# Performance work log

Measured on AMD Instinct MI355X. Metric: run time of the kernel, lower is better.

## Reference

```python
import jax, jax.numpy as jnp
import numpy as np

EPS = 1e-5

def conv3x3(x, w, b):
    # x: [B,C,H,W], w: [O,I,3,3], padding=1 (SAME)
    y = jax.lax.conv_general_dilated(x, w, window_strides=(1, 1),
                                     padding=[(1, 1), (1, 1)],
                                     dimension_numbers=('NCHW', 'OIHW', 'NCHW'))
    return y + b[None, :, None, None]

def pool_block(x, k):
    # exact adaptive avg pool: 300 is divisible by the output size, block size k
    B, C, H, W = x.shape
    return x.reshape(B, C, H // k, k, W // k, k).mean(axis=(3, 5))

def upsample_nearest(x, k):
    # equivalent to the nested python-loop slice-assign in RIA
    return jnp.repeat(jnp.repeat(x, k, axis=2), k, axis=3)

def _conv_param(key, o, i):
    k1, k2 = jax.random.split(key)
    fan_in = i * 9
    w = jax.random.normal(k1, (o, i, 3, 3), jnp.float32) * np.sqrt(2.0 / fan_in)
    b = jax.random.normal(k2, (o,), jnp.float32) * 0.01
    return w, b

def setup_inputs() -> dict:
    key = jax.random.key(0)
    ks = jax.random.split(key, 16)
    inp = {}
    inp['im'] = jax.random.normal(ks[0], (32, 3, 300, 300), jnp.float32)
    inp['w1'], inp['b1'] = _conv_param(ks[1], 8, 3)
    inp['w2'], inp['b2'] = _conv_param(ks[2], 16, 8)
    inp['w3'], inp['b3'] = _conv_param(ks[3], 32, 16)
    inp['w4'], inp['b4'] = _conv_param(ks[4], 16, 32)
    inp['w5'], inp['b5'] = _conv_param(ks[5], 8, 16)
    inp['wc5'], inp['bc5'] = _conv_param(ks[6], 8, 16)
    inp['wc10'], inp['bc10'] = _conv_param(ks[7], 8, 16)
    inp['wc15'], inp['bc15'] = _conv_param(ks[8], 8, 16)
    inp['wg'], inp['bg'] = _conv_param(ks[9], 8, 24)
    inp['wm'], inp['bm'] = _conv_param(ks[10], 8, 24)
    inp['bn_w'] = jnp.ones((8,), jnp.float32)
    inp['bn_b'] = jnp.zeros((8,), jnp.float32)
    inp['w11'], inp['b11'] = _conv_param(ks[11], 1, 8)
    inp['gamma'] = jnp.full((1,), 0.3, jnp.float32)
    return inp

def reference(im, w1, b1, w2, b2, w3, b3, w4, b4, w5, b5,
              wc5, bc5, wc10, bc10, wc15, bc15,
              wg, bg, wm, bm, bn_w, bn_b, w11, b11, gamma):
    # attention conv chain 3->8->16->32->16->8
    x = conv3x3(im, w1, b1)
    x = conv3x3(x, w2, b2)
    x = conv3x3(x, w3, b3)
    x = conv3x3(x, w4, b4)
    x = conv3x3(x, w5, b5)  # [B,8,300,300]

    # RIA: triple-scale pooled context, nearest-upsampled and fused
    up5 = upsample_nearest(pool_block(x, 5), 5)
    up10 = upsample_nearest(pool_block(x, 10), 10)
    up15 = upsample_nearest(pool_block(x, 15), 15)
    c5 = conv3x3(jnp.concatenate([x, up5], axis=1), wc5, bc5)
    c10 = conv3x3(jnp.concatenate([x, up10], axis=1), wc10, bc10)
    c15 = conv3x3(jnp.concatenate([x, up15], axis=1), wc15, bc15)
    g_in = jnp.concatenate([c5, c10, c15], axis=1)  # [B,24,300,300]

    # gated conv (activation=None): conv(x) * sigmoid(mask_conv(x)), then BN (batch stats)
    gated = conv3x3(g_in, wg, bg) * jax.nn.sigmoid(conv3x3(g_in, wm, bm))
    mean = gated.mean(axis=(0, 2, 3), keepdims=True)
    var = gated.var(axis=(0, 2, 3), keepdims=True)
    gated = (gated - mean) * jax.lax.rsqrt(var + EPS)
    gated = gated * bn_w[None, :, None, None] + bn_b[None, :, None, None]

    # 8->1 conv, sigmoid attention map, residual gating with gamma
    att = jax.nn.sigmoid(conv3x3(gated, w11, b11))  # [B,1,300,300]
    out = gamma * (att * im) + (1.0 - gamma) * im
    return out
```

## Files before the change

kernel.cpp:

```cpp
#include <hip/hip_runtime.h>
#include <hip/hip_bf16.h>
#include <math.h>

typedef __hip_bfloat16 bf16;
typedef __attribute__((ext_vector_type(8))) __bf16 bf16x8;
typedef __attribute__((ext_vector_type(8))) unsigned short u16x8;
typedef __attribute__((ext_vector_type(4))) float f32x4;

#define H_ 300
#define W_ 300
#define HW_ 90000
#define NBATCH 32
#define NPART (NBATCH * 190)
#define NPB 95

__device__ __forceinline__ float b2f(unsigned short u) {
    return __uint_as_float((unsigned int)u << 16);
}
__device__ __forceinline__ unsigned short f2u(float v) {
    bf16 b = __float2bfloat16(v);
    return *reinterpret_cast<unsigned short*>(&b);
}
__device__ __forceinline__ float sigm(float x) { return 1.f / (1.f + __expf(-x)); }
__device__ __forceinline__ unsigned int packbf(float a, float b) {
    unsigned int r;
    asm("v_cvt_pk_bf16_f32 %0, %1, %2" : "=v"(r) : "v"(a), "v"(b));
    return r;
}
__device__ __forceinline__ void async_cp16(void* lds_base, const void* g) {
    __builtin_amdgcn_global_load_lds(
        (const __attribute__((address_space(1))) unsigned int*)g,
        (__attribute__((address_space(3))) unsigned int*)lds_base, 16, 0, 0);
}

__global__ void pack_all_k(
    const float* __restrict__ w1, const float* __restrict__ w2,
    const float* __restrict__ w3, const float* __restrict__ w4,
    const float* __restrict__ w5, const float* __restrict__ wc5,
    const float* __restrict__ wc10, const float* __restrict__ wc15,
    const float* __restrict__ wg, const float* __restrict__ wm,
    unsigned short* __restrict__ WP)
{
    const float *a = nullptr, *bsec = nullptr;
    int cs = 999, CO = 0, CI = 0, CP = 8, NS = 3, NG = 1, off = 0, special = 0;
    switch (blockIdx.x) {
        case 0: a = w2;  CO = 16; CI = 8;  CP = 8;  NS = 3; off = 0;     break;
        case 1: a = w3;  CO = 32; CI = 16; CP = 16; NS = 5; NG = 2; off = 2048;  break;
        case 2: a = w4;  CO = 16; CI = 32; CP = 32; NS = 9; off = 8192;  break;
        case 3: a = w5;  CO = 8;  CI = 16; CP = 16; NS = 5; off = 13312; break;
        case 4: special = 1; CO = 32; CI = 32; CP = 32; NS = 9; NG = 2;
                off = 16384; break;
        case 5: a = wg; bsec = wm; cs = 8; CO = 16; CI = 24; CP = 32; NS = 9;
                off = 25600; break;
        case 6: a = w1;  CO = 8;  CI = 3;  CP = 8;  NS = 3; off = 30720; break;
    }
    unsigned short* outp = WP + off;
    int TPK = 32 / CP;
    int total = NS * NG * 512;
    for (int idx = threadIdx.x; idx < total; idx += 256) {
        int j = idx & 7;
        int lane = (idx >> 3) & 63;
        int g = (idx >> 9) % NG;
        int s = idx / (512 * NG);
        int col = lane & 15, kg = lane >> 4;
        int kk = kg * 8 + j;
        int tt = kk / CP, ci = kk % CP;
        int tap = s * TPK + tt;
        float v = 0.f;
        if (special) {
            int o = ci >> 3, c8 = ci & 7;
            int convid = (g == 0) ? (col < 8 ? 0 : 1) : (col < 8 ? 2 : -1);
            if (tap < 9 && convid >= 0) {
                const float* wc = (convid == 0) ? wc5 : (convid == 1) ? wc10 : wc15;
                int colc = col & 7;
                if (o == 0) v = wc[(colc * 16 + c8) * 9 + tap];
                else if (o == convid + 1) v = wc[(colc * 16 + 8 + c8) * 9 + tap];
            }
        } else {
            int co = g * 16 + col;
            if (tap < 9 && ci < CI && co < CO)
                v = (co >= cs) ? bsec[((co - cs) * CI + ci) * 9 + tap]
                               : a[(co * CI + ci) * 9 + tap];
        }
        outp[idx] = f2u(v);
    }
}

template <int CIN, int CINP, int COUT, int NGI, int MODE, int TH>
__global__ __launch_bounds__(256) void mfconv_k(
    const unsigned short* __restrict__ src,
    const unsigned short* __restrict__ wpack,
    const float* __restrict__ bias0, const float* __restrict__ bias1,
    unsigned short* __restrict__ out, int co_total, int co_off,
    float2* __restrict__ bnp, int img_base)
{
    constexpr int TPK = 32 / CINP;
    constexpr int NSTEP = (9 + TPK - 1) / TPK;
    constexpr int OCT = CINP / 8;
    constexpr int NPX = (TH + 2) * 34;
    constexpr int STRIDE = 256 / OCT;

    __shared__ __align__(16) unsigned short s_in[OCT * NPX * 8];

    int b = blockIdx.z;
    int x0 = blockIdx.x * 32, y0 = blockIdx.y * TH;
    int tid = threadIdx.x;
    int lane = tid & 63, wv = tid >> 6;
    bool interior = (x0 >= 1) && (x0 + 32 < W_) && (y0 >= 1) && (y0 + TH < H_);

    int oct = (OCT == 1) ? 0 : (wv % OCT);
    int phase = (OCT == 4) ? 0 : (wv / OCT);
    bool voct = (CIN == CINP) || (oct * 8 < CIN);

    if (MODE == 3) {
        const float* sf = reinterpret_cast<const float*>(src) + (size_t)b * 3 * HW_;
        if (interior) {
            const float* sf0 = sf + (size_t)(y0 - 1) * W_ + (x0 - 1);
            for (int e = tid; e < NPX; e += 256) {
                int y = e / 34;
                size_t o = (size_t)e + (size_t)y * 266;
                u16x8 v = {0, 0, 0, 0, 0, 0, 0, 0};
                v[0] = f2u(sf0[o]);
                v[1] = f2u(sf0[HW_ + o]);
                v[2] = f2u(sf0[2 * HW_ + o]);
                *(u16x8*)&s_in[e * 8] = v;
            }
        } else {
            for (int e = tid; e < NPX; e += 256) {
                int y = e / 34, x = e - y * 34;
                int gy = y0 + y - 1, gx = x0 + x - 1;
                u16x8 v = {0, 0, 0, 0, 0, 0, 0, 0};
                if (gy >= 0 && gy < H_ && gx >= 0 && gx < W_) {
                    size_t o = (size_t)gy * W_ + gx;
                    v[0] = f2u(sf[o]);
                    v[1] = f2u(sf[HW_ + o]);
                    v[2] = f2u(sf[2 * HW_ + o]);
                }
                *(u16x8*)&s_in[e * 8] = v;
            }
        }
    } else {
        const unsigned short* sb = src + (size_t)b * CIN * HW_;
        if (interior) {
            if (voct) {
                const unsigned short* sb0 =
                    sb + ((size_t)(y0 - 1) * W_ + (x0 - 1)) * CIN + oct * 8;
#pragma unroll
                for (int pxb = 0; pxb < NPX; pxb += STRIDE) {
                    int base = phase * 64 + pxb;
                    if (base >= NPX) break;
                    int px = base + lane;
                    if (px < NPX) {
                        int y = px / 34;
                        async_cp16(&s_in[(oct * NPX + base) * 8],
                                   &sb0[(size_t)(px + y * 266) * CIN]);
                    }
                }
            } else {
                u16x8 z8 = {0, 0, 0, 0, 0, 0, 0, 0};
                for (int px = lane + phase * 64; px < NPX; px += STRIDE)
                    *(u16x8*)&s_in[(oct * NPX + px) * 8] = z8;
            }
        } else {
            for (int px = lane + phase * 64; px < NPX; px += STRIDE) {
                int y = px / 34, x = px - y * 34;
                int gy = y0 + y - 1, gx = x0 + x - 1;
                u16x8 v = {0, 0, 0, 0, 0, 0, 0, 0};
                if (gy >= 0 && gy < H_ && gx >= 0 && gx < W_ && voct)
                    v = *(const u16x8*)&sb[((size_t)gy * W_ + gx) * CIN + oct * 8];
                *(u16x8*)&s_in[(oct * NPX + px) * 8] = v;
            }
        }
    }

    bf16x8 bw[NGI][NSTEP];
#pragma unroll
    for (int gi = 0; gi < NGI; ++gi)
#pragma unroll
        for (int s = 0; s < NSTEP; ++s)
            bw[gi][s] = *(const bf16x8*)&wpack[((s * NGI + gi) * 64 + lane) * 8];

    int col = lane & 15, kg = lane >> 4;

    float bias_r[NGI][4];
#pragma unroll
    for (int gi = 0; gi < NGI; ++gi)
#pragma unroll
        for (int r = 0; r < 4; ++r) {
            if (MODE == 2)
                bias_r[0][r] = (kg < 2) ? bias0[kg * 4 + r] : bias1[(kg - 2) * 4 + r];
            else {
                int co_l = gi * 16 + kg * 4 + r;
                bias_r[gi][r] = (co_l < COUT) ? bias0[co_l] : 0.f;
            }
        }

    float bs[4] = {0.f, 0.f, 0.f, 0.f}, bs2[4] = {0.f, 0.f, 0.f, 0.f};

    __syncthreads();

    if constexpr (OCT == 4) {
        int myb = wv * (TH / 4);
#pragma unroll
        for (int tx = 0; tx < 2; ++tx) {
            int pbase = kg * NPX + tx * 16 + col;
            bf16x8 fr[3][3];
#pragma unroll
            for (int r = 0; r < 2; ++r)
#pragma unroll
                for (int dx = 0; dx < 3; ++dx)
                    fr[r][dx] =
                        *(const bf16x8*)&s_in[(pbase + (myb + r) * 34 + dx) * 8];
#pragma unroll
            for (int ii = 0; ii < TH / 4; ++ii) {
#pragma unroll
                for (int dx = 0; dx < 3; ++dx)
                    fr[(ii + 2) % 3][dx] =
                        *(const bf16x8*)&s_in[(pbase + (myb + ii + 2) * 34 + dx) * 8];

                f32x4 acc[NGI];
#pragma unroll
                for (int gi = 0; gi < NGI; ++gi) acc[gi] = {0.f, 0.f, 0.f, 0.f};
#pragma unroll
                for (int dy = 0; dy < 3; ++dy)
#pragma unroll
                    for (int dx = 0; dx < 3; ++dx) {
                        bf16x8 a = fr[(ii + dy) % 3][dx];
#pragma unroll
                        for (int gi = 0; gi < NGI; ++gi)
                            acc[gi] = __builtin_amdgcn_mfma_f32_16x16x32_bf16(
                                bw[gi][dy * 3 + dx], a, acc[gi], 0, 0, 0);
                    }

                int gy = y0 + myb + ii;
                int gxx = x0 + tx * 16 + col;
                if (gy < H_) {
                    if (MODE == 2) {
                        float v0 = acc[0].x + bias_r[0][0];
                        float v1 = acc[0].y + bias_r[0][1];
                        float v2 = acc[0].z + bias_r[0][2];
                        float v3 = acc[0].w + bias_r[0][3];
                        float m0 = __shfl_xor(v0, 32), m1 = __shfl_xor(v1, 32);
                        float m2 = __shfl_xor(v2, 32), m3 = __shfl_xor(v3, 32);
                        if (kg < 2 && gxx < W_) {
                            float o0 = v0 * sigm(m0), o1 = v1 * sigm(m1);
                            float o2 = v2 * sigm(m2), o3 = v3 * sigm(m3);
                            uint2 st;
                            st.x = packbf(o0, o1);
                            st.y = packbf(o2, o3);
                            *(uint2*)&out[(((size_t)b * HW_ + (size_t)gy * W_ +
                                            gxx) * 8) + kg * 4] = st;
                            bs[0] += o0; bs2[0] += o0 * o0;
                            bs[1] += o1; bs2[1] += o1 * o1;
                            bs[2] += o2; bs2[2] += o2 * o2;
                            bs[3] += o3; bs2[3] += o3 * o3;
                        }
                    } else {
#pragma unroll
                        for (int gi = 0; gi < NGI; ++gi) {
                            int co_g = gi * 16 + kg * 4;
                            if (co_g < COUT && gxx < W_) {
                                uint2 st;
                                st.x = packbf(acc[gi].x + bias_r[gi][0],
                                              acc[gi].y + bias_r[gi][1]);
                                st.y = packbf(acc[gi].z + bias_r[gi][2],
                                              acc[gi].w + bias_r[gi][3]);
                                *(uint2*)&out[((size_t)b * HW_ +
                                               (size_t)gy * W_ + gxx) *
                                                  co_total + co_off + co_g] = st;
                            }
                        }
                    }
                }
            }
        }
    } else {
        int offs[NSTEP];
#pragma unroll
        for (int s = 0; s < NSTEP; ++s) {
            int t = s * TPK + kg / OCT;
            if (t > 8) t = 8;
            offs[s] = ((t / 3) * 34 + (t % 3)) * 8 + (kg % OCT) * (NPX * 8);
        }

#pragma unroll
        for (int i = 0; i < TH / 2; ++i) {
            int m = wv * (TH / 2) + i;
            int my = m >> 1, tx = m & 1;
            int gy = y0 + my;
            if (gy >= H_) continue;
            int base = (my * 34 + tx * 16 + col) * 8;

            f32x4 acc[NGI];
#pragma unroll
            for (int gi = 0; gi < NGI; ++gi) acc[gi] = {0.f, 0.f, 0.f, 0.f};
#pragma unroll
            for (int s = 0; s < NSTEP; ++s) {
                bf16x8 a = *(const bf16x8*)&s_in[base + offs[s]];
#pragma unroll
                for (int gi = 0; gi < NGI; ++gi)
                    acc[gi] = __builtin_amdgcn_mfma_f32_16x16x32_bf16(
                        bw[gi][s], a, acc[gi], 0, 0, 0);
            }

            int gxx = x0 + tx * 16 + col;
#pragma unroll
            for (int gi = 0; gi < NGI; ++gi) {
                int co_g = gi * 16 + kg * 4;
                if (co_g < COUT && gxx < W_) {
                    uint2 st;
                    st.x = packbf(acc[gi].x + bias_r[gi][0],
                                  acc[gi].y + bias_r[gi][1]);
                    st.y = packbf(acc[gi].z + bias_r[gi][2],
                                  acc[gi].w + bias_r[gi][3]);
                    *(uint2*)&out[((size_t)b * HW_ + (size_t)gy * W_ + gxx) *
                                      co_total + co_off + co_g] = st;
                }
            }
        }
    }

    if constexpr (MODE == 2) {
#pragma unroll
        for (int off = 1; off < 16; off <<= 1) {
#pragma unroll
            for (int r = 0; r < 4; ++r) {
                bs[r] += __shfl_xor(bs[r], off);
                bs2[r] += __shfl_xor(bs2[r], off);
            }
        }
        __shared__ float bsum[4][8], bsq[4][8];
        if (lane == 0) {
#pragma unroll
            for (int r = 0; r < 4; ++r) { bsum[wv][r] = bs[r]; bsq[wv][r] = bs2[r]; }
        }
        if (lane == 16) {
#pragma unroll
            for (int r = 0; r < 4; ++r) {
                bsum[wv][4 + r] = bs[r];
                bsq[wv][4 + r] = bs2[r];
            }
        }
        __syncthreads();
        if (tid < 8) {
            float s = 0.f, s2 = 0.f;
#pragma unroll
            for (int w = 0; w < 4; ++w) { s += bsum[w][tid]; s2 += bsq[w][tid]; }
            int bIdx = (img_base + b) * 190 + blockIdx.y * 10 + blockIdx.x;
            bnp[(size_t)bIdx * 8 + tid] = make_float2(s, s2);
        }
    }
}

__global__ __launch_bounds__(256) void convc3_k(
    const unsigned short* __restrict__ src,
    const unsigned short* __restrict__ p5, const unsigned short* __restrict__ p10,
    const unsigned short* __restrict__ p15,
    const unsigned short* __restrict__ wpack,
    const float* __restrict__ bc5, const float* __restrict__ bc10,
    const float* __restrict__ bc15, unsigned short* __restrict__ out)
{
    constexpr int TH = 16;
    constexpr int NPX = (TH + 2) * 34;
    __shared__ __align__(16) unsigned short s_in[4 * NPX * 8];

    int b = blockIdx.z;
    int x0 = blockIdx.x * 32, y0 = blockIdx.y * TH;
    int tid = threadIdx.x;
    int lane = tid & 63, wv = tid >> 6;
    bool interior = (x0 >= 1) && (x0 + 32 < W_) && (y0 >= 1) && (y0 + TH < H_);

    const unsigned short* sb = src + (size_t)b * 8 * HW_;
    const unsigned short* pb5 = p5 + (size_t)b * 8 * 3600;
    const unsigned short* pb10 = p10 + (size_t)b * 8 * 900;
    const unsigned short* pb15 = p15 + (size_t)b * 8 * 400;

    int oct = wv;
    if (interior) {
        if (oct == 0) {
            const unsigned short* sb0 =
                sb + ((size_t)(y0 - 1) * W_ + (x0 - 1)) * 8;
#pragma unroll
            for (int base = 0; base < NPX; base += 64) {
                int px = base + lane;
                if (px < NPX) {
                    int y = px / 34;
                    async_cp16(&s_in[(size_t)base * 8],
                               &sb0[(size_t)(px + y * 266) * 8]);
                }
            }
        } else {
            for (int px = lane; px < NPX; px += 64) {
                int y = px / 34, x = px - y * 34;
                int gy = y0 - 1 + y, gx = x0 - 1 + x;
                const unsigned short* pp =
                    (oct == 1) ? &pb5[((size_t)(gy / 5) * 60 + gx / 5) * 8]
                    : (oct == 2) ? &pb10[((size_t)(gy / 10) * 30 + gx / 10) * 8]
                                 : &pb15[((size_t)(gy / 15) * 20 + gx / 15) * 8];
                *(u16x8*)&s_in[(oct * NPX + px) * 8] = *(const u16x8*)pp;
            }
        }
    } else {
        for (int px = lane; px < NPX; px += 64) {
            int y = px / 34, x = px - y * 34;
            int gy = y0 + y - 1, gx = x0 + x - 1;
            u16x8 v = {0, 0, 0, 0, 0, 0, 0, 0};
            if (gy >= 0 && gy < H_ && gx >= 0 && gx < W_) {
                if (oct == 0)
                    v = *(const u16x8*)&sb[((size_t)gy * W_ + gx) * 8];
                else if (oct == 1)
                    v = *(const u16x8*)&pb5[((size_t)(gy / 5) * 60 + gx / 5) * 8];
                else if (oct == 2)
                    v = *(const u16x8*)&pb10[((size_t)(gy / 10) * 30 + gx / 10) * 8];
                else
                    v = *(const u16x8*)&pb15[((size_t)(gy / 15) * 20 + gx / 15) * 8];
            }
            *(u16x8*)&s_in[(oct * NPX + px) * 8] = v;
        }
    }

    bf16x8 bw[2][9];
#pragma unroll
    for (int g = 0; g < 2; ++g)
#pragma unroll
        for (int s = 0; s < 9; ++s)
            bw[g][s] = *(const bf16x8*)&wpack[((s * 2 + g) * 64 + lane) * 8];

    int col = lane & 15, kg = lane >> 4;
    float bias_r[2][4];
#pragma unroll
    for (int r = 0; r < 4; ++r) {
        bias_r[0][r] = (kg < 2) ? bc5[kg * 4 + r] : bc10[(kg - 2) * 4 + r];
        bias_r[1][r] = (kg < 2) ? bc15[kg * 4 + r] : 0.f;
    }

    __syncthreads();

    int myb = wv * (TH / 4);
#pragma unroll
    for (int tx = 0; tx < 2; ++tx) {
        int pbase = kg * NPX + tx * 16 + col;
        bf16x8 fr[3][3];
#pragma unroll
        for (int r = 0; r < 2; ++r)
#pragma unroll
            for (int dx = 0; dx < 3; ++dx)
                fr[r][dx] = *(const bf16x8*)&s_in[(pbase + (myb + r) * 34 + dx) * 8];
#pragma unroll
        for (int ii = 0; ii < TH / 4; ++ii) {
#pragma unroll
            for (int dx = 0; dx < 3; ++dx)
                fr[(ii + 2) % 3][dx] =
                    *(const bf16x8*)&s_in[(pbase + (myb + ii + 2) * 34 + dx) * 8];

            f32x4 acc[2];
            acc[0] = {0.f, 0.f, 0.f, 0.f};
            acc[1] = {0.f, 0.f, 0.f, 0.f};
#pragma unroll
            for (int dy = 0; dy < 3; ++dy)
#pragma unroll
                for (int dx = 0; dx < 3; ++dx) {
                    bf16x8 a = fr[(ii + dy) % 3][dx];
                    acc[0] = __builtin_amdgcn_mfma_f32_16x16x32_bf16(
                        bw[0][dy * 3 + dx], a, acc[0], 0, 0, 0);
                    acc[1] = __builtin_amdgcn_mfma_f32_16x16x32_bf16(
                        bw[1][dy * 3 + dx], a, acc[1], 0, 0, 0);
                }

            int gy = y0 + myb + ii;
            int gxx = x0 + tx * 16 + col;
            if (gy < H_ && gxx < W_) {
                size_t pxo = ((size_t)b * HW_ + (size_t)gy * W_ + gxx) * 24;
                uint2 st0;
                st0.x = packbf(acc[0].x + bias_r[0][0], acc[0].y + bias_r[0][1]);
                st0.y = packbf(acc[0].z + bias_r[0][2], acc[0].w + bias_r[0][3]);
                *(uint2*)&out[pxo + kg * 4] = st0;
                if (kg < 2) {
                    uint2 st1;
                    st1.x = packbf(acc[1].x + bias_r[1][0], acc[1].y + bias_r[1][1]);
                    st1.y = packbf(acc[1].z + bias_r[1][2], acc[1].w + bias_r[1][3]);
                    *(uint2*)&out[pxo + 16 + kg * 4] = st1;
                }
            }
        }
    }
}

__global__ __launch_bounds__(256) void pool5_k(const unsigned short* __restrict__ x,
                                               unsigned short* __restrict__ p5,
                                               int n)
{
    int idx = blockIdx.x * 256 + threadIdx.x;
    if (idx >= n) return;
    int b = idx / 3600;
    int rem = idx - b * 3600;
    int i = rem / 60, j = rem - i * 60;
    const unsigned short* src =
        x + ((size_t)b * HW_ + (size_t)(i * 5) * W_ + j * 5) * 8;
    float ss[8] = {0, 0, 0, 0, 0, 0, 0, 0};
#pragma unroll
    for (int r = 0; r < 5; ++r)
#pragma unroll
        for (int c = 0; c < 5; ++c) {
            u16x8 v = *(const u16x8*)&src[((size_t)r * W_ + c) * 8];
#pragma unroll
            for (int k = 0; k < 8; ++k) ss[k] += b2f(v[k]);
        }
    uint4 st;
    st.x = packbf(ss[0] * 0.04f, ss[1] * 0.04f);
    st.y = packbf(ss[2] * 0.04f, ss[3] * 0.04f);
    st.z = packbf(ss[4] * 0.04f, ss[5] * 0.04f);
    st.w = packbf(ss[6] * 0.04f, ss[7] * 0.04f);
    *(uint4*)&p5[(size_t)idx * 8] = st;
}

template <int R, int OD>
__device__ __forceinline__ void poolr_body(const unsigned short* __restrict__ p5,
                                           unsigned short* __restrict__ po, int idx)
{
    int b = idx / (OD * OD);
    int rem = idx - b * OD * OD;
    int i = rem / OD, j = rem - i * OD;
    const unsigned short* src =
        p5 + ((size_t)b * 3600 + (size_t)(i * R) * 60 + j * R) * 8;
    float ss[8] = {0, 0, 0, 0, 0, 0, 0, 0};
    const float inv = 1.f / (R * R);
#pragma unroll
    for (int r = 0; r < R; ++r)
#pragma unroll
        for (int c = 0; c < R; ++c) {
            u16x8 v = *(const u16x8*)&src[((size_t)r * 60 + c) * 8];
#pragma unroll
            for (int k = 0; k < 8; ++k) ss[k] += b2f(v[k]);
        }
    uint4 st;
    st.x = packbf(ss[0] * inv, ss[1] * inv);
    st.y = packbf(ss[2] * inv, ss[3] * inv);
    st.z = packbf(ss[4] * inv, ss[5] * inv);
    st.w = packbf(ss[6] * inv, ss[7] * inv);
    *(uint4*)&po[(size_t)idx * 8] = st;
}

__global__ __launch_bounds__(256) void poolrs_k(const unsigned short* __restrict__ p5,
                                                unsigned short* __restrict__ p10,
                                                unsigned short* __restrict__ p15,
                                                int n10, int n15)
{
    int idx = blockIdx.x * 256 + threadIdx.x;
    if (idx < n10) {
        poolr_body<2, 30>(p5, p10, idx);
    } else {
        idx -= n10;
        if (idx < n15) poolr_body<3, 20>(p5, p15, idx);
    }
}

__global__ __launch_bounds__(256) void reduce_parts_k(
    const float2* __restrict__ parts, float2* __restrict__ parts2)
{
    int k = blockIdx.x;
    int tid = threadIdx.x;
    int c = tid & 7, j = tid >> 3;
    float s = 0.f, s2 = 0.f;
    for (int r = j; r < NPB; r += 32) {
        float2 p = parts[((size_t)k * NPB + r) * 8 + c];
        s += p.x;
        s2 += p.y;
    }
    __shared__ float2 red[256];
    red[tid] = make_float2(s, s2);
    __syncthreads();
    if (tid < 8) {
        float a = 0.f, b = 0.f;
        for (int q = 0; q < 32; ++q) {
            float2 p = red[q * 8 + tid];
            a += p.x;
            b += p.y;
        }
        parts2[(size_t)k * 8 + tid] = make_float2(a, b);
    }
}

__global__ __launch_bounds__(256) void stats_fold_k(
    const float2* __restrict__ parts2, const float* __restrict__ bn_w,
    const float* __restrict__ bn_b, const float* __restrict__ w11,
    const float* __restrict__ b11, float* __restrict__ wfold)
{
    __shared__ float sc[8], tc[8];
    __shared__ float2 acc8[8];
    int tid = threadIdx.x;
    int c = tid >> 5, sl = tid & 31;
    float s = 0.f, s2 = 0.f;
    for (int i = sl; i < 64; i += 32) {
        float2 p = parts2[(size_t)i * 8 + c];
        s += p.x;
        s2 += p.y;
    }
#pragma unroll
    for (int off = 16; off > 0; off >>= 1) {
        s += __shfl_down(s, off, 32);
        s2 += __shfl_down(s2, off, 32);
    }
    if (sl == 0) acc8[c] = make_float2(s, s2);
    __syncthreads();
    if (tid < 8) {
        double ds = acc8[tid].x, ds2 = acc8[tid].y;
        double N = (double)NBATCH * HW_;
        double mean = ds / N;
        double var = ds2 / N - mean * mean;
        float rstd = (float)(1.0 / sqrt(var + 1e-5));
        float scv = bn_w[tid] * rstd;
        sc[tid] = scv;
        tc[tid] = bn_b[tid] - (float)mean * scv;
    }
    __syncthreads();
    if (tid < 72) {
        int t = tid >> 3, ci = tid & 7;
        wfold[tid] = w11[ci * 9 + t] * sc[ci];
    }
    if (tid == 72) {
        float a = b11[0];
        for (int i = 0; i < 72; ++i) a += w11[i] * tc[i / 9];
        wfold[72] = a;
    }
}

__global__ __launch_bounds__(256) void final_k(
    const unsigned short* __restrict__ gated, const float* __restrict__ wf,
    const float* __restrict__ im, const float* __restrict__ gamma,
    float* __restrict__ out)
{
    __shared__ __align__(16) unsigned short s_g[1156 * 8];
    __shared__ float s_w[80];

    int b = blockIdx.z;
    int x0 = blockIdx.x * 32, y0 = blockIdx.y * 32;
    int tid = threadIdx.x;
    bool interior = (x0 >= 1) && (x0 + 32 < W_) && (y0 >= 1) && (y0 + 32 < H_);

    if (tid < 73) s_w[tid] = wf[tid];

    const unsigned short* gb = gated + (size_t)b * HW_ * 8;
    if (interior) {
        const unsigned short* gb0 = gb + ((size_t)(y0 - 1) * W_ + (x0 - 1)) * 8;
        for (int e = tid; e < 1156; e += 256) {
            int y = e / 34;
            u16x8 v = *(const u16x8*)&gb0[(size_t)(e + y * 266) * 8];
            *(u16x8*)&s_g[e * 8] = v;
        }
    } else {
        for (int e = tid; e < 1156; e += 256) {
            int y = e / 34, x = e - y * 34;
            int gy = y0 + y - 1, gx = x0 + x - 1;
            u16x8 v = {0, 0, 0, 0, 0, 0, 0, 0};
            if (gy >= 0 && gy < H_ && gx >= 0 && gx < W_)
                v = *(const u16x8*)&gb[((size_t)gy * W_ + gx) * 8];
            *(u16x8*)&s_g[e * 8] = v;
        }
    }
    __syncthreads();

    int qx = (tid & 15) * 2, qy = (tid >> 4) * 2;
    float f[4];
    float gm = *gamma;
#pragma unroll
    for (int p = 0; p < 4; ++p) {
        int ly = qy + (p >> 1), lx = qx + (p & 1);
        float acc = s_w[72];
#pragma unroll
        for (int t = 0; t < 9; ++t) {
            u16x8 n = *(const u16x8*)&s_g[((ly + t / 3) * 34 + lx + t % 3) * 8];
#pragma unroll
            for (int ci = 0; ci < 8; ++ci) acc += b2f(n[ci]) * s_w[t * 8 + ci];
        }
        f[p] = (1.f - gm) + gm * sigm(acc);
    }

    int px = x0 + qx, py = y0 + qy;
    if (px < W_) {
#pragma unroll
        for (int ch = 0; ch < 3; ++ch) {
            const float* imb = im + ((size_t)b * 3 + ch) * HW_;
            float* ob = out + ((size_t)b * 3 + ch) * HW_;
#pragma unroll
            for (int pr = 0; pr < 2; ++pr) {
                if (py + pr < H_) {
                    float2 iv = *(const float2*)&imb[(size_t)(py + pr) * W_ + px];
                    float2 ov;
                    ov.x = iv.x * f[pr * 2 + 0];
                    ov.y = iv.y * f[pr * 2 + 1];
                    *(float2*)&ob[(size_t)(py + pr) * W_ + px] = ov;
                }
            }
        }
    }
}


extern "C" void kernel_launch(void* const* d_in, const int* in_sizes, int n_in,
                              void* d_out, int out_size, void* d_ws,
                              size_t ws_size, hipStream_t stream)
{
    (void)in_sizes; (void)n_in; (void)out_size;

    const float* im  = (const float*)d_in[0];
    const float* w1  = (const float*)d_in[1];
    const float* b1  = (const float*)d_in[2];
    const float* w2  = (const float*)d_in[3];
    const float* b2  = (const float*)d_in[4];
    const float* w3  = (const float*)d_in[5];
    const float* b3  = (const float*)d_in[6];
    const float* w4  = (const float*)d_in[7];
    const float* b4  = (const float*)d_in[8];
    const float* w5  = (const float*)d_in[9];
    const float* b5  = (const float*)d_in[10];
    const float* wc5 = (const float*)d_in[11];
    const float* bc5 = (const float*)d_in[12];
    const float* wc10= (const float*)d_in[13];
    const float* bc10= (const float*)d_in[14];
    const float* wc15= (const float*)d_in[15];
    const float* bc15= (const float*)d_in[16];
    const float* wg  = (const float*)d_in[17];
    const float* bg  = (const float*)d_in[18];
    const float* wm  = (const float*)d_in[19];
    const float* bm  = (const float*)d_in[20];
    const float* bnw = (const float*)d_in[21];
    const float* bnb = (const float*)d_in[22];
    const float* w11 = (const float*)d_in[23];
    const float* b11 = (const float*)d_in[24];
    const float* gam = (const float*)d_in[25];
    float* out = (float*)d_out;

    const size_t GATED_B = 46080000;
    const size_t PER_IMG = 1440000 + 2880000 + 5760000 + 57600 + 14400 + 6656;
    const size_t MISC    = 1048576;
    int c = 32;
    while (c > 1 && GATED_B + MISC + (size_t)c * PER_IMG + 2048 > ws_size)
        c >>= 1;

    char* p = (char*)d_ws;
    auto take = [&](size_t bytes) {
        char* r = p;
        p += (bytes + 255) & ~(size_t)255;
        return r;
    };
    unsigned short* GATED = (unsigned short*)take(GATED_B);
    unsigned short* A   = (unsigned short*)take((size_t)c * 1440000);
    unsigned short* Bb  = (unsigned short*)take((size_t)c * 2880000);
    unsigned short* C   = (unsigned short*)take((size_t)c * 5760000);
    unsigned short* P5  = (unsigned short*)take((size_t)c * 57600);
    unsigned short* P10 = (unsigned short*)take((size_t)c * 14400);
    unsigned short* P15 = (unsigned short*)take((size_t)c * 6656);
    float2* parts  = (float2*)take((size_t)NPART * 8 * sizeof(float2));
    float2* parts2 = (float2*)take(64 * 8 * sizeof(float2));
    float*  wfold  = (float*)take(512);
    unsigned short* WP = (unsigned short*)take(65536);

    unsigned short* PK2 = WP;
    unsigned short* PK3 = WP + 2048;
    unsigned short* PK4 = WP + 8192;
    unsigned short* PK5 = WP + 13312;
    unsigned short* PKc = WP + 16384;
    unsigned short* PKg = WP + 25600;
    unsigned short* PK1 = WP + 30720;

    dim3 blk(256);

    pack_all_k<<<dim3(7), blk, 0, stream>>>(w1, w2, w3, w4, w5, wc5, wc10, wc15,
                                            wg, wm, WP);

    for (int b0 = 0; b0 < NBATCH; b0 += c) {
        dim3 g32(10, 10, c);
        dim3 g16(10, 19, c);
        const float* imc = im + (size_t)b0 * 3 * HW_;

        mfconv_k<8, 8, 8, 1, 3, 32><<<g32, blk, 0, stream>>>(
            (const unsigned short*)imc, PK1, b1, nullptr, A, 8, 0, nullptr, 0);
        mfconv_k<8, 8, 16, 1, 0, 32><<<g32, blk, 0, stream>>>(
            A, PK2, b2, nullptr, Bb, 16, 0, nullptr, 0);
        mfconv_k<16, 16, 32, 2, 0, 32><<<g32, blk, 0, stream>>>(
            Bb, PK3, b3, nullptr, C, 32, 0, nullptr, 0);
        mfconv_k<32, 32, 16, 1, 0, 16><<<g16, blk, 0, stream>>>(
            C, PK4, b4, nullptr, Bb, 16, 0, nullptr, 0);
        mfconv_k<16, 16, 8, 1, 0, 32><<<g32, blk, 0, stream>>>(
            Bb, PK5, b5, nullptr, A, 8, 0, nullptr, 0);

        int n5 = c * 3600, n10 = c * 900, n15 = c * 400;
        pool5_k<<<dim3((n5 + 255) / 256), blk, 0, stream>>>(A, P5, n5);
        poolrs_k<<<dim3((n10 + n15 + 255) / 256), blk, 0, stream>>>(P5, P10, P15,
                                                                    n10, n15);

        convc3_k<<<g16, blk, 0, stream>>>(A, P5, P10, P15, PKc, bc5, bc10, bc15, C);

        mfconv_k<24, 32, 16, 1, 2, 16><<<g16, blk, 0, stream>>>(
            C, PKg, bg, bm, GATED + (size_t)b0 * HW_ * 8, 8, 0, parts, b0);
    }

    reduce_parts_k<<<dim3(64), blk, 0, stream>>>(parts, parts2);
    stats_fold_k<<<dim3(1), blk, 0, stream>>>(parts2, bnw, bnb, w11, b11, wfold);
    final_k<<<dim3(10, 10, NBATCH), blk, 0, stream>>>(GATED, wfold, im, gam,
                                                      out);
}
```

Baseline: 419.1 us.

## Fuse first two convolutions into one kernel and async-load final_k tile

Adds a kernel that computes conv1 (3->8) on a halo-extended 34x34 tile in shared memory and then conv2 (8->16) from it. This removes the intermediate A write and read and one launch per chunk, at the cost of recomputing halo pixels of conv1. It also switches the interior tile load in final_k to async 16-byte copies and drops the now-unused float-input mode from mfconv_k.

```diff
diff --git a/kernel.cpp b/kernel.cpp
--- a/kernel.cpp
+++ b/kernel.cpp
@@ -86,6 +86,127 @@
     }
 }
 
+__global__ __launch_bounds__(256) void fused12_k(
+    const float* __restrict__ im, const unsigned short* __restrict__ wp1,
+    const float* __restrict__ b1, const unsigned short* __restrict__ wp2,
+    const float* __restrict__ b2, unsigned short* __restrict__ out)
+{
+    __shared__ __align__(16) unsigned short s_im[1296 * 8];
+    __shared__ __align__(16) unsigned short s_x1[1156 * 8];
+
+    int b = blockIdx.z;
+    int x0 = blockIdx.x * 32, y0 = blockIdx.y * 32;
+    int tid = threadIdx.x;
+    int lane = tid & 63, wv = tid >> 6;
+    int col = lane & 15, kg = lane >> 4;
+
+    const float* sf = im + (size_t)b * 3 * HW_;
+    bool interior = (x0 >= 2) && (x0 + 34 < W_) && (y0 >= 2) && (y0 + 34 < H_);
+    if (interior) {
+        const float* sf0 = sf + (size_t)(y0 - 2) * W_ + (x0 - 2);
+        for (int e = tid; e < 1296; e += 256) {
+            int y = e / 36;
+            size_t o = (size_t)e + (size_t)y * 264;
+            u16x8 v = {0, 0, 0, 0, 0, 0, 0, 0};
+            v[0] = f2u(sf0[o]);
+            v[1] = f2u(sf0[HW_ + o]);
+            v[2] = f2u(sf0[2 * HW_ + o]);
+            *(u16x8*)&s_im[e * 8] = v;
+        }
+    } else {
+        for (int e = tid; e < 1296; e += 256) {
+            int y = e / 36, x = e - y * 36;
+            int gy = y0 + y - 2, gx = x0 + x - 2;
+            u16x8 v = {0, 0, 0, 0, 0, 0, 0, 0};
+            if (gy >= 0 && gy < H_ && gx >= 0 && gx < W_) {
+                size_t o = (size_t)gy * W_ + gx;
+                v[0] = f2u(sf[o]);
+                v[1] = f2u(sf[HW_ + o]);
+                v[2] = f2u(sf[2 * HW_ + o]);
+            }
+            *(u16x8*)&s_im[e * 8] = v;
+        }
+    }
+
+    bf16x8 bw1[3], bw2[3];
+#pragma unroll
+    for (int s = 0; s < 3; ++s) {
+        bw1[s] = *(const bf16x8*)&wp1[(s * 64 + lane) * 8];
+        bw2[s] = *(const bf16x8*)&wp2[(s * 64 + lane) * 8];
+    }
+
+    int offs1[3], offs2[3];
+#pragma unroll
+    for (int s = 0; s < 3; ++s) {
+        int t = s * 4 + kg;
+        if (t > 8) t = 8;
+        offs1[s] = ((t / 3) * 36 + (t % 3)) * 8;
+        offs2[s] = ((t / 3) * 34 + (t % 3)) * 8;
+    }
+
+    float b1r[4], b2r[4];
+#pragma unroll
+    for (int r = 0; r < 4; ++r) {
+        int co1 = kg * 4 + r;
+        b1r[r] = (co1 < 8) ? b1[co1] : 0.f;
+        b2r[r] = b2[kg * 4 + r];
+    }
+
+    __syncthreads();
+
+    for (int r = wv; r < 34; r += 4) {
+#pragma unroll
+        for (int cg = 0; cg < 3; ++cg) {
+            int base = (r * 36 + cg * 16 + col) * 8;
+            f32x4 acc = {0.f, 0.f, 0.f, 0.f};
+#pragma unroll
+            for (int s = 0; s < 3; ++s) {
+                bf16x8 a = *(const bf16x8*)&s_im[base + offs1[s]];
+                acc = __builtin_amdgcn_mfma_f32_16x16x32_bf16(bw1[s], a, acc, 0, 0, 0);
+            }
+            int c = cg * 16 + col;
+            if (kg < 2 && c < 34) {
+                int gy = y0 - 1 + r, gx = x0 - 1 + c;
+                bool ok = (gy >= 0) && (gy < H_) && (gx >= 0) && (gx < W_);
+                float o0 = ok ? acc.x + b1r[0] : 0.f;
+                float o1 = ok ? acc.y + b1r[1] : 0.f;
+                float o2 = ok ? acc.z + b1r[2] : 0.f;
+                float o3 = ok ? acc.w + b1r[3] : 0.f;
+                uint2 st;
+                st.x = packbf(o0, o1);
+                st.y = packbf(o2, o3);
+                *(uint2*)&s_x1[(r * 34 + c) * 8 + kg * 4] = st;
+            }
+        }
+    }
+    __syncthreads();
+
+#pragma unroll
+    for (int i = 0; i < 16; ++i) {
+        int m = wv * 16 + i;
+        int my = m >> 1, tx = m & 1;
+        int gy = y0 + my;
+        if (gy >= H_) continue;
+        int base = (my * 34 + tx * 16 + col) * 8;
+
+        f32x4 acc = {0.f, 0.f, 0.f, 0.f};
+#pragma unroll
+        for (int s = 0; s < 3; ++s) {
+            bf16x8 a = *(const bf16x8*)&s_x1[base + offs2[s]];
+            acc = __builtin_amdgcn_mfma_f32_16x16x32_bf16(bw2[s], a, acc, 0, 0, 0);
+        }
+
+        int gxx = x0 + tx * 16 + col;
+        if (gxx < W_) {
+            uint2 st;
+            st.x = packbf(acc.x + b2r[0], acc.y + b2r[1]);
+            st.y = packbf(acc.z + b2r[2], acc.w + b2r[3]);
+            *(uint2*)&out[((size_t)b * HW_ + (size_t)gy * W_ + gxx) * 16 +
+                          kg * 4] = st;
+        }
+    }
+}
+
 template <int CIN, int CINP, int COUT, int NGI, int MODE, int TH>
 __global__ __launch_bounds__(256) void mfconv_k(
     const unsigned short* __restrict__ src,
@@ -112,34 +233,7 @@
     int phase = (OCT == 4) ? 0 : (wv / OCT);
     bool voct = (CIN == CINP) || (oct * 8 < CIN);
 
-    if (MODE == 3) {
-        const float* sf = reinterpret_cast<const float*>(src) + (size_t)b * 3 * HW_;
-        if (interior) {
-            const float* sf0 = sf + (size_t)(y0 - 1) * W_ + (x0 - 1);
-            for (int e = tid; e < NPX; e += 256) {
-                int y = e / 34;
-                size_t o = (size_t)e + (size_t)y * 266;
-                u16x8 v = {0, 0, 0, 0, 0, 0, 0, 0};
-                v[0] = f2u(sf0[o]);
-                v[1] = f2u(sf0[HW_ + o]);
-                v[2] = f2u(sf0[2 * HW_ + o]);
-                *(u16x8*)&s_in[e * 8] = v;
-            }
-        } else {
-            for (int e = tid; e < NPX; e += 256) {
-                int y = e / 34, x = e - y * 34;
-                int gy = y0 + y - 1, gx = x0 + x - 1;
-                u16x8 v = {0, 0, 0, 0, 0, 0, 0, 0};
-                if (gy >= 0 && gy < H_ && gx >= 0 && gx < W_) {
-                    size_t o = (size_t)gy * W_ + gx;
-                    v[0] = f2u(sf[o]);
-                    v[1] = f2u(sf[HW_ + o]);
-                    v[2] = f2u(sf[2 * HW_ + o]);
-                }
-                *(u16x8*)&s_in[e * 8] = v;
-            }
-        }
-    } else {
+    {
         const unsigned short* sb = src + (size_t)b * CIN * HW_;
         if (interior) {
             if (voct) {
@@ -636,6 +730,7 @@
     int b = blockIdx.z;
     int x0 = blockIdx.x * 32, y0 = blockIdx.y * 32;
     int tid = threadIdx.x;
+    int lane = tid & 63, wv = tid >> 6;
     bool interior = (x0 >= 1) && (x0 + 32 < W_) && (y0 >= 1) && (y0 + 32 < H_);
 
     if (tid < 73) s_w[tid] = wf[tid];
@@ -643,10 +738,13 @@
     const unsigned short* gb = gated + (size_t)b * HW_ * 8;
     if (interior) {
         const unsigned short* gb0 = gb + ((size_t)(y0 - 1) * W_ + (x0 - 1)) * 8;
-        for (int e = tid; e < 1156; e += 256) {
-            int y = e / 34;
-            u16x8 v = *(const u16x8*)&gb0[(size_t)(e + y * 266) * 8];
-            *(u16x8*)&s_g[e * 8] = v;
+        for (int base = wv * 64; base < 1156; base += 256) {
+            int px = base + lane;
+            if (px < 1156) {
+                int y = px / 34;
+                async_cp16(&s_g[(size_t)base * 8],
+                           &gb0[(size_t)(px + y * 266) * 8]);
+            }
         }
     } else {
         for (int e = tid; e < 1156; e += 256) {
@@ -774,10 +872,8 @@
         dim3 g16(10, 19, c);
         const float* imc = im + (size_t)b0 * 3 * HW_;
 
-        mfconv_k<8, 8, 8, 1, 3, 32><<<g32, blk, 0, stream>>>(
-            (const unsigned short*)imc, PK1, b1, nullptr, A, 8, 0, nullptr, 0);
-        mfconv_k<8, 8, 16, 1, 0, 32><<<g32, blk, 0, stream>>>(
-            A, PK2, b2, nullptr, Bb, 16, 0, nullptr, 0);
+        fused12_k<<<g32, blk, 0, stream>>>(imc, PK1, b1, PK2, b2, Bb);
+
         mfconv_k<16, 16, 32, 2, 0, 32><<<g32, blk, 0, stream>>>(
             Bb, PK3, b3, nullptr, C, 32, 0, nullptr, 0);
         mfconv_k<32, 32, 16, 1, 0, 16><<<g16, blk, 0, stream>>>(
```

Result: no change. 413.1 us (-1.4%).
